# Kernel tuning notes

Hardware: AMD Instinct MI355X
Metric: run time of the kernel (lower is better)

## Reference

```python
import math
import jax, jax.numpy as jnp
import numpy as np

B, CK, H, W = 4, 64, 48, 84


def setup_inputs() -> dict:
    key = jax.random.key(0)
    k1, k2 = jax.random.split(key)
    mk = jax.random.normal(k1, (B, CK, 1, H, W), dtype=jnp.float32)
    qk = jax.random.normal(k2, (B, CK, H, W), dtype=jnp.float32)
    return {"mk": mk, "qk": qk}


def reference(mk, qk):
    b_, ck = mk.shape[0], mk.shape[1]
    mkf = mk.reshape(b_, ck, -1)            # [B, CK, N]  (N = T*H*W, T=1)
    qkf = qk.reshape(b_, ck, -1)            # [B, CK, M]  (M = H*W)
    a = jnp.sum(mkf * mkf, axis=1)[:, :, None]              # [B, N, 1]
    b = 2.0 * jnp.einsum('bcn,bcm->bnm', mkf, qkf)          # [B, N, M]
    c = jnp.sum(qkf * qkf, axis=1)[:, None, :]              # [B, 1, M]
    affinity = (-a + b - c) / math.sqrt(ck)                 # -||mk - qk||^2 / sqrt(CK)
    return jax.nn.softmax(affinity, axis=1)                 # softmax over memory axis
```

## Files before the change

kernel.cpp:

```cpp
#include <hip/hip_runtime.h>
#include <hip/hip_fp16.h>
#include <math.h>

#define B_  4
#define CK_ 64
#define N_  4032
#define M_  4032
#define NP_ 4096
#define MP_ 4096

#define P1C 8
#define P1T 8

typedef __attribute__((ext_vector_type(8))) short short8;
typedef __attribute__((ext_vector_type(4))) float float4v;

__device__ inline unsigned short f2bf(float x) {
    unsigned u = __float_as_uint(x);
    u += 0x7FFF + ((u >> 16) & 1);
    return (unsigned short)(u >> 16);
}
__device__ inline float bf2f(unsigned short h) {
    return __uint_as_float(((unsigned)h) << 16);
}

__global__ __launch_bounds__(256) void prep_kernel(
    const float* __restrict__ mk, const float* __restrict__ qk,
    unsigned short* __restrict__ mk_hi, unsigned short* __restrict__ mk_lo,
    unsigned short* __restrict__ qk_hi, unsigned short* __restrict__ qk_lo,
    float* __restrict__ u, float* __restrict__ v)
{
    __shared__ float tile[64][65];
    __shared__ float sred[4][64];
    const int t  = threadIdx.x;
    const int n0 = blockIdx.x * 64;
    const int b  = blockIdx.y;
    const int which = blockIdx.z;
    const bool pad = (n0 >= N_);

    const float* src = (which == 0 ? mk : qk) + (size_t)b * CK_ * N_;
    unsigned short* dhi = (which == 0 ? mk_hi : qk_hi) + (size_t)b * NP_ * CK_;
    unsigned short* dlo = (which == 0 ? mk_lo : qk_lo) + (size_t)b * NP_ * CK_;

    if (!pad) {
        #pragma unroll
        for (int i = 0; i < 16; ++i) {
            const int idx = t + 256 * i;
            const int c = idx >> 6, n = idx & 63;
            tile[c][n] = src[(size_t)c * N_ + n0 + n];
        }
    } else {
        #pragma unroll
        for (int i = 0; i < 16; ++i) {
            const int idx = t + 256 * i;
            tile[idx >> 6][idx & 63] = 0.f;
        }
    }
    __syncthreads();

    const int n = t & 63;
    const int g = t >> 6;
    unsigned short hbits[16], lbits[16];
    float ssq = 0.f;
    #pragma unroll
    for (int i = 0; i < 16; ++i) {
        const float x = tile[g * 16 + i][n];
        const unsigned short h = f2bf(x);
        hbits[i] = h;
        lbits[i] = f2bf(x - bf2f(h));
        ssq = fmaf(x, x, ssq);
    }
    {
        union { short8 vv; unsigned short s[8]; } p0, p1, q0, q1;
        #pragma unroll
        for (int i = 0; i < 8; ++i) {
            p0.s[i] = hbits[i]; p1.s[i] = hbits[8 + i];
            q0.s[i] = lbits[i]; q1.s[i] = lbits[8 + i];
        }
        const size_t base = (size_t)(n0 + n) * CK_ + g * 16;
        *(short8*)(dhi + base)     = p0.vv;
        *(short8*)(dhi + base + 8) = p1.vv;
        *(short8*)(dlo + base)     = q0.vv;
        *(short8*)(dlo + base + 8) = q1.vv;
    }
    sred[g][n] = ssq;
    __syncthreads();
    if (t < 64) {
        const float tot = sred[0][t] + sred[1][t] + sred[2][t] + sred[3][t];
        float* dst = (which == 0 ? u : v);
        dst[(size_t)b * NP_ + n0 + t] = pad ? 0.f : __expf(-0.125f * tot);
    }
}


__global__ __launch_bounds__(512) void pass1_kernel(
    const unsigned short* __restrict__ mk_hi, const unsigned short* __restrict__ mk_lo,
    const unsigned short* __restrict__ qk_hi, const unsigned short* __restrict__ qk_lo,
    const float* __restrict__ u, const float* __restrict__ v,
    float* __restrict__ psum, float* __restrict__ out)
{
    __shared__ float cs[2][128];
    const int t = threadIdx.x;
    const int wave = t >> 6, lane = t & 63;
    const int wn = wave & 1, wm = wave >> 1;
    const int lcol = lane & 15;
    const int quad = lane >> 4;
    const int chunk = blockIdx.y;
    const int b = blockIdx.z;
    const int m_base = blockIdx.x * 128 + wm * 32;

    const unsigned short* mh = mk_hi + (size_t)b * NP_ * CK_;
    const unsigned short* ml = mk_lo + (size_t)b * NP_ * CK_;
    const unsigned short* qh = qk_hi + (size_t)b * NP_ * CK_;
    const unsigned short* ql = qk_lo + (size_t)b * NP_ * CK_;
    const float* ub = u + (size_t)b * NP_;

    short8 qah[2][2], qal[2][2];
    #pragma unroll
    for (int mg = 0; mg < 2; ++mg) {
        const size_t mrow = (size_t)(m_base + mg * 16 + lcol) * CK_;
        #pragma unroll
        for (int kc = 0; kc < 2; ++kc) {
            const size_t off = mrow + kc * 32 + quad * 8;
            qah[mg][kc] = *(const short8*)(qh + off);
            qal[mg][kc] = *(const short8*)(ql + off);
        }
    }

    float4v vv[2];
    #pragma unroll
    for (int mg = 0; mg < 2; ++mg)
        vv[mg] = *(const float4v*)(v + (size_t)b * NP_ + m_base + mg * 16 + quad * 4);

    const bool mv0 = (m_base < N_);
    const bool mv1 = (m_base + 16 < N_);

    unsigned short* wb = (unsigned short*)(out + (size_t)b * N_ * M_);

    float ps[2][4];
    #pragma unroll
    for (int mg = 0; mg < 2; ++mg)
        #pragma unroll
        for (int r = 0; r < 4; ++r) ps[mg][r] = 0.f;

    #pragma unroll 2
    for (int it = chunk * P1T; it < chunk * P1T + P1T; ++it) {
        const int n_base = it * 64 + wn * 32;

        short8 bh[2][2], bl[2][2];
        #pragma unroll
        for (int ng = 0; ng < 2; ++ng) {
            const size_t nrow = (size_t)(n_base + ng * 16 + lcol) * CK_;
            #pragma unroll
            for (int kc = 0; kc < 2; ++kc) {
                const size_t off = nrow + kc * 32 + quad * 8;
                bh[ng][kc] = *(const short8*)(mh + off);
                bl[ng][kc] = *(const short8*)(ml + off);
            }
        }
        float un_[2];
        #pragma unroll
        for (int ng = 0; ng < 2; ++ng)
            un_[ng] = ub[n_base + ng * 16 + lcol];

        const bool nv0 = (n_base < N_);
        const bool nv1 = (n_base + 16 < N_);

        #pragma unroll
        for (int mg = 0; mg < 2; ++mg) {
            #pragma unroll
            for (int ng = 0; ng < 2; ++ng) {
                float4v a1 = {0.f, 0.f, 0.f, 0.f};
                float4v a2 = {0.f, 0.f, 0.f, 0.f};
                __builtin_amdgcn_s_setprio(1);
                #pragma unroll
                for (int kc = 0; kc < 2; ++kc) {
                    a1 = __builtin_amdgcn_mfma_f32_16x16x32_bf16(qah[mg][kc], bh[ng][kc], a1, 0, 0, 0);
                    a2 = __builtin_amdgcn_mfma_f32_16x16x32_bf16(qah[mg][kc], bl[ng][kc], a2, 0, 0, 0);
                    a2 = __builtin_amdgcn_mfma_f32_16x16x32_bf16(qal[mg][kc], bh[ng][kc], a2, 0, 0, 0);
                }
                __builtin_amdgcn_s_setprio(0);
                float4v wv;
                #pragma unroll
                for (int r = 0; r < 4; ++r) {
                    const float dot = a1[r] + a2[r];
                    wv[r] = un_[ng] * __expf(0.25f * dot) * vv[mg][r];
                    ps[mg][r] += wv[r];
                }
                if ((ng == 0 ? nv0 : nv1) && (mg == 0 ? mv0 : mv1)) {
                    __half2 hA = __floats2half2_rn(wv[0], wv[1]);
                    __half2 hB = __floats2half2_rn(wv[2], wv[3]);
                    uint2 pk;
                    pk.x = *(unsigned*)&hA;
                    pk.y = *(unsigned*)&hB;
                    *(uint2*)(wb + (size_t)(n_base + ng * 16 + lcol) * (2 * M_)
                                  + m_base + mg * 16 + quad * 4) = pk;
                }
            }
        }
    }

    #pragma unroll
    for (int mg = 0; mg < 2; ++mg)
        #pragma unroll
        for (int r = 0; r < 4; ++r) {
            float s = ps[mg][r];
            s += __shfl_xor(s, 1);
            s += __shfl_xor(s, 2);
            s += __shfl_xor(s, 4);
            s += __shfl_xor(s, 8);
            ps[mg][r] = s;
        }
    if (lcol == 0) {
        #pragma unroll
        for (int mg = 0; mg < 2; ++mg)
            #pragma unroll
            for (int r = 0; r < 4; ++r)
                cs[wn][wm * 32 + mg * 16 + quad * 4 + r] = ps[mg][r];
    }
    __syncthreads();
    if (t < 128) {
        psum[((size_t)b * P1C + chunk) * MP_ + blockIdx.x * 128 + t] =
            cs[0][t] + cs[1][t];
    }
}

__global__ __launch_bounds__(256) void reduce_kernel(
    const float* __restrict__ psum, float* __restrict__ rinv)
{
    const int m = blockIdx.x * 256 + threadIdx.x;
    const int b = blockIdx.y;
    float s = 0.f;
    #pragma unroll
    for (int c = 0; c < P1C; ++c)
        s += psum[((size_t)b * P1C + c) * MP_ + m];
    rinv[(size_t)b * MP_ + m] = 1.f / s;
}

__global__ __launch_bounds__(256) void pass2_kernel(
    const float* __restrict__ rinv, float* __restrict__ out)
{
    const int t = threadIdx.x;
    const int n = blockIdx.x;
    const int b = blockIdx.y;
    float* row = out + ((size_t)b * N_ + n) * M_;
    const unsigned short* wr = (const unsigned short*)row;
    const float* rv = rinv + (size_t)b * MP_;

    const int c0 = t;
    const int c1 = t + 256;
    const bool has1 = (c1 < (M_ / 8));

    uint4 q0 = *(const uint4*)(wr + c0 * 8);
    float4v ra0 = *(const float4v*)(rv + c0 * 8);
    float4v rb0 = *(const float4v*)(rv + c0 * 8 + 4);
    uint4 q1;
    float4v ra1, rb1;
    if (has1) {
        q1  = *(const uint4*)(wr + c1 * 8);
        ra1 = *(const float4v*)(rv + c1 * 8);
        rb1 = *(const float4v*)(rv + c1 * 8 + 4);
    }

    float4v xa0, xb0, xa1, xb1;
    {
        float2 f0 = __half22float2(*(const __half2*)&q0.x);
        float2 f1 = __half22float2(*(const __half2*)&q0.y);
        float2 f2 = __half22float2(*(const __half2*)&q0.z);
        float2 f3 = __half22float2(*(const __half2*)&q0.w);
        xa0 = (float4v){f0.x * ra0[0], f0.y * ra0[1], f1.x * ra0[2], f1.y * ra0[3]};
        xb0 = (float4v){f2.x * rb0[0], f2.y * rb0[1], f3.x * rb0[2], f3.y * rb0[3]};
    }
    if (has1) {
        float2 f0 = __half22float2(*(const __half2*)&q1.x);
        float2 f1 = __half22float2(*(const __half2*)&q1.y);
        float2 f2 = __half22float2(*(const __half2*)&q1.z);
        float2 f3 = __half22float2(*(const __half2*)&q1.w);
        xa1 = (float4v){f0.x * ra1[0], f0.y * ra1[1], f1.x * ra1[2], f1.y * ra1[3]};
        xb1 = (float4v){f2.x * rb1[0], f2.y * rb1[1], f3.x * rb1[2], f3.y * rb1[3]};
    }

    asm volatile("s_waitcnt vmcnt(0)" ::: "memory");
    __syncthreads();

    __builtin_nontemporal_store(xa0, (float4v*)(row + c0 * 8));
    __builtin_nontemporal_store(xb0, (float4v*)(row + c0 * 8 + 4));
    if (has1) {
        __builtin_nontemporal_store(xa1, (float4v*)(row + c1 * 8));
        __builtin_nontemporal_store(xb1, (float4v*)(row + c1 * 8 + 4));
    }
}

extern "C" void kernel_launch(void* const* d_in, const int* in_sizes, int n_in,
                              void* d_out, int out_size, void* d_ws, size_t ws_size,
                              hipStream_t stream) {
    const float* mk = (const float*)d_in[0];
    const float* qk = (const float*)d_in[1];
    float* out = (float*)d_out;

    unsigned short* mk_hi = (unsigned short*)d_ws;
    unsigned short* mk_lo = mk_hi + (size_t)B_ * NP_ * CK_;
    unsigned short* qk_hi = mk_lo + (size_t)B_ * NP_ * CK_;
    unsigned short* qk_lo = qk_hi + (size_t)B_ * NP_ * CK_;
    float* u    = (float*)(qk_lo + (size_t)B_ * NP_ * CK_);
    float* v    = u + (size_t)B_ * NP_;
    float* psum = v + (size_t)B_ * NP_;
    float* rinv = psum + (size_t)B_ * P1C * MP_;

    prep_kernel<<<dim3(NP_ / 64, B_, 2), 256, 0, stream>>>(mk, qk, mk_hi, mk_lo, qk_hi, qk_lo, u, v);
    pass1_kernel<<<dim3(MP_ / 128, P1C, B_), 512, 0, stream>>>(mk_hi, mk_lo, qk_hi, qk_lo, u, v, psum, out);
    reduce_kernel<<<dim3(MP_ / 256, B_), 256, 0, stream>>>(psum, rinv);
    pass2_kernel<<<dim3(N_, B_), 256, 0, stream>>>(rinv, out);
}
```

Before: 382.1 us.

## Stage pass1 fp16 tiles in LDS for coalesced nontemporal row stores

Pass1 now writes each wave's fp16 exp weights into a double-buffered shared-memory tile, then after a block barrier it emits full 32-byte contiguous row segments with nontemporal stores. Previously each lane scattered 8-byte stores straight to global memory. The exponent is also folded into one exp of (dot/4 - a - c), with padding handled by a large norm value instead of per-store validity checks. The cost is one __syncthreads per iteration and the LDS traffic, and the old unroll-2 pragma is removed.

```diff
diff --git a/kernel.cpp b/kernel.cpp
--- a/kernel.cpp
+++ b/kernel.cpp
@@ -14,6 +14,8 @@
 
 typedef __attribute__((ext_vector_type(8))) short short8;
 typedef __attribute__((ext_vector_type(4))) float float4v;
+typedef __attribute__((ext_vector_type(4))) unsigned int uint4v;
+typedef __attribute__((ext_vector_type(2))) unsigned int uint2v;
 
 __device__ inline unsigned short f2bf(float x) {
     unsigned u = __float_as_uint(x);
@@ -23,12 +25,23 @@
 __device__ inline float bf2f(unsigned short h) {
     return __uint_as_float(((unsigned)h) << 16);
 }
+__device__ inline float2 h2u_to_f2(unsigned v) {
+    __half2 h;
+    __builtin_memcpy(&h, &v, 4);
+    return __half22float2(h);
+}
+__device__ inline unsigned f2_to_h2u(float a, float b) {
+    __half2 h = __floats2half2_rn(a, b);
+    unsigned u;
+    __builtin_memcpy(&u, &h, 4);
+    return u;
+}
 
 __global__ __launch_bounds__(256) void prep_kernel(
     const float* __restrict__ mk, const float* __restrict__ qk,
     unsigned short* __restrict__ mk_hi, unsigned short* __restrict__ mk_lo,
     unsigned short* __restrict__ qk_hi, unsigned short* __restrict__ qk_lo,
-    float* __restrict__ u, float* __restrict__ v)
+    float* __restrict__ eu, float* __restrict__ ev)
 {
     __shared__ float tile[64][65];
     __shared__ float sred[4][64];
@@ -87,8 +100,8 @@
     __syncthreads();
     if (t < 64) {
         const float tot = sred[0][t] + sred[1][t] + sred[2][t] + sred[3][t];
-        float* dst = (which == 0 ? u : v);
-        dst[(size_t)b * NP_ + n0 + t] = pad ? 0.f : __expf(-0.125f * tot);
+        float* dst = (which == 0 ? eu : ev);
+        dst[(size_t)b * NP_ + n0 + t] = pad ? 1e30f : 0.125f * tot;
     }
 }
 
@@ -96,9 +109,10 @@
 __global__ __launch_bounds__(512) void pass1_kernel(
     const unsigned short* __restrict__ mk_hi, const unsigned short* __restrict__ mk_lo,
     const unsigned short* __restrict__ qk_hi, const unsigned short* __restrict__ qk_lo,
-    const float* __restrict__ u, const float* __restrict__ v,
+    const float* __restrict__ eu, const float* __restrict__ ev,
     float* __restrict__ psum, float* __restrict__ out)
 {
+    __shared__ unsigned short wt[2][64][136];
     __shared__ float cs[2][128];
     const int t = threadIdx.x;
     const int wave = t >> 6, lane = t & 63;
@@ -107,13 +121,14 @@
     const int quad = lane >> 4;
     const int chunk = blockIdx.y;
     const int b = blockIdx.z;
-    const int m_base = blockIdx.x * 128 + wm * 32;
+    const int m_blk  = blockIdx.x * 128;
+    const int m_base = m_blk + wm * 32;
 
     const unsigned short* mh = mk_hi + (size_t)b * NP_ * CK_;
     const unsigned short* ml = mk_lo + (size_t)b * NP_ * CK_;
     const unsigned short* qh = qk_hi + (size_t)b * NP_ * CK_;
     const unsigned short* ql = qk_lo + (size_t)b * NP_ * CK_;
-    const float* ub = u + (size_t)b * NP_;
+    const float* eub = eu + (size_t)b * NP_;
 
     short8 qah[2][2], qal[2][2];
     #pragma unroll
@@ -127,13 +142,10 @@
         }
     }
 
-    float4v vv[2];
+    float4v ev4[2];
     #pragma unroll
     for (int mg = 0; mg < 2; ++mg)
-        vv[mg] = *(const float4v*)(v + (size_t)b * NP_ + m_base + mg * 16 + quad * 4);
-
-    const bool mv0 = (m_base < N_);
-    const bool mv1 = (m_base + 16 < N_);
+        ev4[mg] = *(const float4v*)(ev + (size_t)b * NP_ + m_base + mg * 16 + quad * 4);
 
     unsigned short* wb = (unsigned short*)(out + (size_t)b * N_ * M_);
 
@@ -143,7 +155,11 @@
         #pragma unroll
         for (int r = 0; r < 4; ++r) ps[mg][r] = 0.f;
 
-    #pragma unroll 2
+    const int crow = t >> 3;
+    const int cseg = t & 7;
+    const bool mseg_ok = (m_blk + cseg * 16) < N_;
+
+    int p = 0;
     for (int it = chunk * P1T; it < chunk * P1T + P1T; ++it) {
         const int n_base = it * 64 + wn * 32;
 
@@ -158,13 +174,10 @@
                 bl[ng][kc] = *(const short8*)(ml + off);
             }
         }
-        float un_[2];
+        float eun[2];
         #pragma unroll
         for (int ng = 0; ng < 2; ++ng)
-            un_[ng] = ub[n_base + ng * 16 + lcol];
-
-        const bool nv0 = (n_base < N_);
-        const bool nv1 = (n_base + 16 < N_);
+            eun[ng] = eub[n_base + ng * 16 + lcol];
 
         #pragma unroll
         for (int mg = 0; mg < 2; ++mg) {
@@ -184,20 +197,31 @@
                 #pragma unroll
                 for (int r = 0; r < 4; ++r) {
                     const float dot = a1[r] + a2[r];
-                    wv[r] = un_[ng] * __expf(0.25f * dot) * vv[mg][r];
+                    const float x = fmaf(dot, 0.25f, -eun[ng] - ev4[mg][r]);
+                    wv[r] = __expf(x);
                     ps[mg][r] += wv[r];
                 }
-                if ((ng == 0 ? nv0 : nv1) && (mg == 0 ? mv0 : mv1)) {
-                    __half2 hA = __floats2half2_rn(wv[0], wv[1]);
-                    __half2 hB = __floats2half2_rn(wv[2], wv[3]);
-                    uint2 pk;
-                    pk.x = *(unsigned*)&hA;
-                    pk.y = *(unsigned*)&hB;
-                    *(uint2*)(wb + (size_t)(n_base + ng * 16 + lcol) * (2 * M_)
-                                  + m_base + mg * 16 + quad * 4) = pk;
-                }
+                const unsigned ua = f2_to_h2u(wv[0], wv[1]);
+                const unsigned ub = f2_to_h2u(wv[2], wv[3]);
+                uint2v pk;
+                pk.x = ua;
+                pk.y = ub;
+                const int n_rel = wn * 32 + ng * 16 + lcol;
+                const int m_rel = wm * 32 + mg * 16 + quad * 4;
+                *(uint2v*)&wt[p][n_rel][m_rel] = pk;
             }
         }
+        __syncthreads();
+
+        const int n_g = it * 64 + crow;
+        if (n_g < N_ && mseg_ok) {
+            const uint4v* s = (const uint4v*)&wt[p][crow][cseg * 16];
+            uint4v v0 = s[0], v1 = s[1];
+            unsigned short* dst = wb + (size_t)n_g * (2 * M_) + m_blk + cseg * 16;
+            __builtin_nontemporal_store(v0, (uint4v*)dst);
+            __builtin_nontemporal_store(v1, (uint4v*)(dst + 8));
+        }
+        p ^= 1;
     }
 
     #pragma unroll
@@ -251,31 +275,31 @@
     const int c1 = t + 256;
     const bool has1 = (c1 < (M_ / 8));
 
-    uint4 q0 = *(const uint4*)(wr + c0 * 8);
+    uint4v q0 = *(const uint4v*)(wr + c0 * 8);
     float4v ra0 = *(const float4v*)(rv + c0 * 8);
     float4v rb0 = *(const float4v*)(rv + c0 * 8 + 4);
-    uint4 q1;
+    uint4v q1;
     float4v ra1, rb1;
     if (has1) {
-        q1  = *(const uint4*)(wr + c1 * 8);
+        q1  = *(const uint4v*)(wr + c1 * 8);
         ra1 = *(const float4v*)(rv + c1 * 8);
         rb1 = *(const float4v*)(rv + c1 * 8 + 4);
     }
 
     float4v xa0, xb0, xa1, xb1;
     {
-        float2 f0 = __half22float2(*(const __half2*)&q0.x);
-        float2 f1 = __half22float2(*(const __half2*)&q0.y);
-        float2 f2 = __half22float2(*(const __half2*)&q0.z);
-        float2 f3 = __half22float2(*(const __half2*)&q0.w);
+        float2 f0 = h2u_to_f2(q0.x);
+        float2 f1 = h2u_to_f2(q0.y);
+        float2 f2 = h2u_to_f2(q0.z);
+        float2 f3 = h2u_to_f2(q0.w);
         xa0 = (float4v){f0.x * ra0[0], f0.y * ra0[1], f1.x * ra0[2], f1.y * ra0[3]};
         xb0 = (float4v){f2.x * rb0[0], f2.y * rb0[1], f3.x * rb0[2], f3.y * rb0[3]};
     }
     if (has1) {
-        float2 f0 = __half22float2(*(const __half2*)&q1.x);
-        float2 f1 = __half22float2(*(const __half2*)&q1.y);
-        float2 f2 = __half22float2(*(const __half2*)&q1.z);
-        float2 f3 = __half22float2(*(const __half2*)&q1.w);
+        float2 f0 = h2u_to_f2(q1.x);
+        float2 f1 = h2u_to_f2(q1.y);
+        float2 f2 = h2u_to_f2(q1.z);
+        float2 f3 = h2u_to_f2(q1.w);
         xa1 = (float4v){f0.x * ra1[0], f0.y * ra1[1], f1.x * ra1[2], f1.y * ra1[3]};
         xb1 = (float4v){f2.x * rb1[0], f2.y * rb1[1], f3.x * rb1[2], f3.y * rb1[3]};
     }
@@ -302,13 +326,13 @@
     unsigned short* mk_lo = mk_hi + (size_t)B_ * NP_ * CK_;
     unsigned short* qk_hi = mk_lo + (size_t)B_ * NP_ * CK_;
     unsigned short* qk_lo = qk_hi + (size_t)B_ * NP_ * CK_;
-    float* u    = (float*)(qk_lo + (size_t)B_ * NP_ * CK_);
-    float* v    = u + (size_t)B_ * NP_;
-    float* psum = v + (size_t)B_ * NP_;
+    float* eu   = (float*)(qk_lo + (size_t)B_ * NP_ * CK_);
+    float* ev   = eu + (size_t)B_ * NP_;
+    float* psum = ev + (size_t)B_ * NP_;
     float* rinv = psum + (size_t)B_ * P1C * MP_;
 
-    prep_kernel<<<dim3(NP_ / 64, B_, 2), 256, 0, stream>>>(mk, qk, mk_hi, mk_lo, qk_hi, qk_lo, u, v);
-    pass1_kernel<<<dim3(MP_ / 128, P1C, B_), 512, 0, stream>>>(mk_hi, mk_lo, qk_hi, qk_lo, u, v, psum, out);
+    prep_kernel<<<dim3(NP_ / 64, B_, 2), 256, 0, stream>>>(mk, qk, mk_hi, mk_lo, qk_hi, qk_lo, eu, ev);
+    pass1_kernel<<<dim3(MP_ / 128, P1C, B_), 512, 0, stream>>>(mk_hi, mk_lo, qk_hi, qk_lo, eu, ev, psum, out);
     reduce_kernel<<<dim3(MP_ / 256, B_), 256, 0, stream>>>(psum, rinv);
     pass2_kernel<<<dim3(N_, B_), 256, 0, stream>>>(rinv, out);
 }
```

Measured after the change: 407.4 us. +6.6%, slower.
